# Performance work log

Hardware: AMD Instinct MI355X
Metric: run time of the kernel (lower is better)

The kernel has to match this reference:

```python
import jax, jax.numpy as jnp
import numpy as np


def setup_inputs() -> dict:
    key = jax.random.key(0)
    ks = jax.random.split(key, 8)
    B, C, N = 4, 64, 32768
    d = C // 8
    inp = {
        "x": jax.random.normal(ks[0], (B, C, N), dtype=jnp.float32),
        "Wq": jax.random.normal(ks[1], (d, C), dtype=jnp.float32) * 0.1,
        "bq": jax.random.normal(ks[2], (d,), dtype=jnp.float32) * 0.1,
        "Wk": jax.random.normal(ks[3], (d, C), dtype=jnp.float32) * 0.1,
        "bk": jax.random.normal(ks[4], (d,), dtype=jnp.float32) * 0.1,
        "Wv": jax.random.normal(ks[5], (C, C), dtype=jnp.float32) * 0.1,
        "bv": jax.random.normal(ks[6], (C,), dtype=jnp.float32) * 0.1,
        # nn.Parameter(torch.zeros(1)) in the original; nonzero here so the
        # attention branch actually contributes to the output.
        "gamma": jax.random.normal(ks[7], (1,), dtype=jnp.float32) * 0.1,
        "window_size": 512,
        "stride": 256,
        "pooling_factor": 2,
    }
    return inp


def reference(x, Wq, bq, Wk, bk, Wv, bv, gamma, window_size, stride, pooling_factor):
    B, C, N = x.shape
    # conv1x1 projections are pointwise -> apply once on the full signal
    q = jnp.einsum("dc,bcn->bdn", Wq, x) + bq[None, :, None]  # [B, d, N]
    k = jnp.einsum("dc,bcn->bdn", Wk, x) + bk[None, :, None]  # [B, d, N]
    v = jnp.einsum("ec,bcn->ben", Wv, x) + bv[None, :, None]  # [B, C, N]

    starts = jnp.arange(0, N - window_size + 1, stride)              # [W]
    idx = starts[:, None] + jnp.arange(window_size)[None, :]         # [W, ws]

    qw = q[:, :, idx]  # [B, d, W, ws]
    kw = k[:, :, idx]
    vw = v[:, :, idx]  # [B, C, W, ws]
    xw = x[:, :, idx]

    energy = jnp.einsum("bdwi,bdwj->bwij", qw, kw)                   # [B, W, ws, ws]
    attn = jax.nn.softmax(energy, axis=-1)
    # torch: bmm(v, attn^T) -> out[c,i] = sum_j v[c,j] * attn[i,j]
    out_local = jnp.einsum("bcwj,bwij->bcwi", vw, attn)              # [B, C, W, ws]

    contrib = gamma[0] * out_local + xw
    out = jnp.zeros_like(x).at[:, :, idx].add(contrib)               # overlap-add
    counts = jnp.zeros((N,), x.dtype).at[idx].add(1.0)               # overlap count
    out = out / counts[None, None, :]

    P = pooling_factor
    Np = (N // P) * P
    out = out[:, :, :Np].reshape(B, C, N // P, P).max(axis=-1)       # MaxPool1d(P)
    return out
```

## Files before the change

### kernel.cpp

```cpp
#include <hip/hip_runtime.h>
#include <hip/hip_bf16.h>

#define BB 4
#define CC 64
#define DD 8
#define NN 32768
#define WW 512
#define STR 256
#define NWIN 127
#define LOG2E 1.4426950408889634f

typedef short bf16x8 __attribute__((ext_vector_type(8)));
typedef float f32x4 __attribute__((ext_vector_type(4)));
typedef float f32x16 __attribute__((ext_vector_type(16)));

__device__ __forceinline__ unsigned int pack_bf16(float lo, float hi) {
    __hip_bfloat162 h = __float22bfloat162_rn(make_float2(lo, hi));
    unsigned int r; __builtin_memcpy(&r, &h, 4);
    return r;
}
__device__ __forceinline__ unsigned short to_bf16(float f) {
    __hip_bfloat16 h = __float2bfloat16(f);
    unsigned short r; __builtin_memcpy(&r, &h, 2);
    return r;
}
__device__ __forceinline__ float bf2f(unsigned short s) {
    union { unsigned int u; float f; } v; v.u = ((unsigned int)s) << 16;
    return v.f;
}
__device__ __forceinline__ float fast_exp2(float x) {
#if __has_builtin(__builtin_amdgcn_exp2f)
    return __builtin_amdgcn_exp2f(x);
#else
    float r; asm("v_exp_f32 %0, %1" : "=v"(r) : "v"(x)); return r;
#endif
}
__device__ __forceinline__ void plswap(unsigned int &x, unsigned int &y) {
    asm("v_permlane32_swap_b32 %0, %1" : "+v"(x), "+v"(y));
}
__device__ __forceinline__ bf16x8 pack8(float a0, float a1, float a2, float a3,
                                        float a4, float a5, float a6, float a7) {
    union { bf16x8 v; unsigned int u[4]; } r;
    r.u[0] = pack_bf16(a0, a1); r.u[1] = pack_bf16(a2, a3);
    r.u[2] = pack_bf16(a4, a5); r.u[3] = pack_bf16(a6, a7);
    return r.v;
}
__device__ __forceinline__ bf16x8 words4(unsigned int w0, unsigned int w1,
                                         unsigned int w2, unsigned int w3) {
    union { bf16x8 v; unsigned int u[4]; } r;
    r.u[0] = w0; r.u[1] = w1; r.u[2] = w2; r.u[3] = w3;
    return r.v;
}


__global__ __launch_bounds__(256) void qkv_kernel(
    const float* __restrict__ x,
    const float* __restrict__ Wq, const float* __restrict__ bq,
    const float* __restrict__ Wk, const float* __restrict__ bk,
    const float* __restrict__ Wv, const float* __restrict__ bv,
    unsigned short* __restrict__ qout, unsigned short* __restrict__ kout,
    unsigned short* __restrict__ vout)
{
    const int t = threadIdx.x;
    const int lane = t & 63, wv = t >> 6;
    const int a = lane & 15, g = lane >> 4;

    bf16x8 wf[5][2];
    #pragma unroll
    for (int T = 0; T < 5; ++T) {
        const float* wrow;
        float scale = 1.f;
        if (T == 0) {
            if (a < 8) { wrow = Wq + a*CC; scale = LOG2E; }
            else       { wrow = Wk + (a-8)*CC; }
        } else {
            wrow = Wv + ((T-1)*16 + a)*CC;
        }
        #pragma unroll
        for (int h = 0; h < 2; ++h) {
            float4 w0 = *(const float4*)(wrow + h*32 + g*8);
            float4 w1 = *(const float4*)(wrow + h*32 + g*8 + 4);
            wf[T][h] = pack8(w0.x*scale, w0.y*scale, w0.z*scale, w0.w*scale,
                             w1.x*scale, w1.y*scale, w1.z*scale, w1.w*scale);
        }
    }
    f32x4 bias[5];
    {
        const int r = g*4;
        #pragma unroll
        for (int u = 0; u < 4; ++u) {
            int rr = r + u;
            bias[0][u] = (rr < 8) ? bq[rr]*LOG2E : bk[rr-8];
        }
        #pragma unroll
        for (int T = 1; T < 5; ++T)
            #pragma unroll
            for (int u = 0; u < 4; ++u)
                bias[T][u] = bv[(T-1)*16 + r + u];
    }

    const int wave_id = blockIdx.x*4 + wv;
    #pragma unroll 1
    for (int it = 0; it < 2; ++it) {
        const int chunk = wave_id + it*4096;
        const int b = chunk >> 11;
        const int n0 = (chunk & 2047) * 16;
        const int n = n0 + a;
        const float* xcol = x + (size_t)b*CC*NN + n;

        float xv0[8], xv1[8];
        #pragma unroll
        for (int u = 0; u < 8; ++u) xv0[u] = xcol[(size_t)(g*8 + u)*NN];
        #pragma unroll
        for (int u = 0; u < 8; ++u) xv1[u] = xcol[(size_t)(32 + g*8 + u)*NN];
        bf16x8 xb0 = pack8(xv0[0],xv0[1],xv0[2],xv0[3],xv0[4],xv0[5],xv0[6],xv0[7]);
        bf16x8 xb1 = pack8(xv1[0],xv1[1],xv1[2],xv1[3],xv1[4],xv1[5],xv1[6],xv1[7]);

        f32x4 acc[5];
        #pragma unroll
        for (int T = 0; T < 5; ++T) {
            acc[T] = __builtin_amdgcn_mfma_f32_16x16x32_bf16(wf[T][0], xb0, bias[T], 0, 0, 0);
            acc[T] = __builtin_amdgcn_mfma_f32_16x16x32_bf16(wf[T][1], xb1, acc[T], 0, 0, 0);
        }

        {
            unsigned int lo = pack_bf16(acc[0][0], acc[0][1]);
            unsigned int hi = pack_bf16(acc[0][2], acc[0][3]);
            unsigned short* base = ((g < 2) ? qout : kout) + ((size_t)b*NN + n)*8 + (g & 1)*4;
            *(int2*)base = make_int2((int)lo, (int)hi);
        }
        unsigned short* vtb = vout + (((size_t)b*1024 + (n>>5))*4 + ((n>>3)&3))*512 + (n&7);
        #pragma unroll
        for (int T = 1; T < 5; ++T) {
            #pragma unroll
            for (int u = 0; u < 4; ++u) {
                const int e = (T-1)*16 + g*4 + u;
                vtb[e*8] = to_bf16(acc[T][u]);
            }
        }
    }
}

__global__ __launch_bounds__(128, 4) void attn_kernel(
    const unsigned short* __restrict__ qg, const unsigned short* __restrict__ kg,
    const unsigned short* __restrict__ vg,
    unsigned short* __restrict__ accE, unsigned short* __restrict__ accO)
{
    const int t = threadIdx.x;
    const int lane = t & 63, wv = t >> 6;
    const int l31 = lane & 31, hi = lane >> 5;
    int bid = (blockIdx.x & 7)*508 + (blockIdx.x >> 3);
    const int oct = bid & 7; bid >>= 3;
    const int w = bid % NWIN, b = bid / NWIN;
    const int nwin = STR * w;
    const int i0 = oct*64 + wv*32;

    const unsigned short* qbase = qg + ((size_t)b*NN + nwin + i0)*8;
    const unsigned short* kbase = kg + ((size_t)b*NN + nwin)*8;
    const unsigned short* vt = vg + (((size_t)b*1024 + 8*w)*4 + 2*hi)*512 + (size_t)l31*8;

    const bf16x8 zf = {};
    bf16x8 qf;
    {
        bf16x8 raw = *(const bf16x8*)(qbase + (size_t)l31*8);
        qf = hi ? zf : raw;
    }

    f32x16 acc[2] = {};
    float2 rsum2 = make_float2(0.f, 0.f);

    bf16x8 kc = *(const bf16x8*)(kbase + (size_t)l31*8);

    #pragma unroll 2
    for (int jt = 0; jt < 16; ++jt) {
        bf16x8 kn = kc;
        if (jt < 15) kn = *(const bf16x8*)(kbase + (size_t)(jt*32 + 32 + l31)*8);
        bf16x8 vc[2][2];
        #pragma unroll
        for (int ct = 0; ct < 2; ++ct)
            #pragma unroll
            for (int sl = 0; sl < 2; ++sl)
                vc[ct][sl] = *(const bf16x8*)(vt + (size_t)(jt*4 + sl*2)*512 + ct*256);

        const f32x16 z16 = {};
        f32x16 E = __builtin_amdgcn_mfma_f32_32x32x16_bf16(kc, qf, z16, 0, 0, 0);
        #pragma unroll
        for (int r = 0; r < 16; ++r) E[r] = fast_exp2(E[r]);
        float2 s0 = make_float2(E[0],  E[1])  + make_float2(E[2],  E[3]);
        float2 s1 = make_float2(E[4],  E[5])  + make_float2(E[6],  E[7]);
        float2 s2 = make_float2(E[8],  E[9])  + make_float2(E[10], E[11]);
        float2 s3 = make_float2(E[12], E[13]) + make_float2(E[14], E[15]);
        rsum2 += (s0 + s1) + (s2 + s3);
        unsigned int wd[8];
        #pragma unroll
        for (int tw = 0; tw < 8; ++tw) wd[tw] = pack_bf16(E[2*tw], E[2*tw+1]);
        unsigned int F0 = wd[0], F2 = wd[2]; plswap(F0, F2);
        unsigned int F1 = wd[1], F3 = wd[3]; plswap(F1, F3);
        unsigned int G0 = wd[4], G2 = wd[6]; plswap(G0, G2);
        unsigned int G1 = wd[5], G3 = wd[7]; plswap(G1, G3);
        bf16x8 pa0 = words4(F0, F1, F2, F3);
        bf16x8 pa1 = words4(G0, G1, G2, G3);
        #pragma unroll
        for (int ct = 0; ct < 2; ++ct) {
            acc[ct] = __builtin_amdgcn_mfma_f32_32x32x16_bf16(pa0, vc[ct][0], acc[ct], 0, 0, 0);
            acc[ct] = __builtin_amdgcn_mfma_f32_32x32x16_bf16(pa1, vc[ct][1], acc[ct], 0, 0, 0);
        }
        kc = kn;
    }

    float r = rsum2.x + rsum2.y;
    r += __shfl_xor(r, 32);
    const float inv = 1.f / r;
    f32x4 invv[4];
    #pragma unroll
    for (int g = 0; g < 4; ++g)
        #pragma unroll
        for (int u = 0; u < 4; ++u)
            invv[g][u] = __shfl(inv, 8*g + 4*hi + u);

    unsigned short* ob = ((w & 1) ? accO : accE)
        + ((size_t)b*1024 + ((nwin + i0) >> 5))*4*512 + 4*hi;
    #pragma unroll
    for (int ct = 0; ct < 2; ++ct) {
        unsigned short* cbase = ob + (ct*32 + l31)*8;
        #pragma unroll
        for (int g = 0; g < 4; ++g) {
            float a0 = acc[ct][4*g+0] * invv[g][0];
            float a1 = acc[ct][4*g+1] * invv[g][1];
            float a2 = acc[ct][4*g+2] * invv[g][2];
            float a3 = acc[ct][4*g+3] * invv[g][3];
            int2 pw = make_int2((int)pack_bf16(a0, a1), (int)pack_bf16(a2, a3));
            *(int2*)(cbase + (size_t)g*512) = pw;
        }
    }
}

__global__ __launch_bounds__(256) void final_kernel(
    const float* __restrict__ x,
    const unsigned short* __restrict__ accE, const unsigned short* __restrict__ accO,
    const float* __restrict__ gamma, float* __restrict__ out)
{
    const size_t tid = (size_t)blockIdx.x*256 + threadIdx.x;
    const size_t base = tid*8;
    const int n = (int)(base & (NN-1));
    const int c = (int)((base >> 15) & (CC-1));
    const int b = (int)(base >> 21);
    const float g = gamma[0];
    const size_t tadr = (((size_t)b*1024 + (n >> 5))*4 + ((n >> 3) & 3))*512 + c*8;

    float xv[8];
    *(float4*)&xv[0] = *(const float4*)&x[base];
    *(float4*)&xv[4] = *(const float4*)&x[base+4];
    int4 aeq = *(const int4*)&accE[tadr];
    const unsigned int* ae = (const unsigned int*)&aeq;

    float s[8];
    if (n >= STR && n < NN - STR) {
        int4 aoq = *(const int4*)&accO[tadr];
        const unsigned int* ao = (const unsigned int*)&aoq;
        #pragma unroll
        for (int u = 0; u < 4; ++u) {
            float e0 = bf2f((unsigned short)(ae[u] & 0xffff));
            float e1 = bf2f((unsigned short)(ae[u] >> 16));
            float o0 = bf2f((unsigned short)(ao[u] & 0xffff));
            float o1 = bf2f((unsigned short)(ao[u] >> 16));
            s[2*u]   = fmaf(g, (e0 + o0)*0.5f, xv[2*u]);
            s[2*u+1] = fmaf(g, (e1 + o1)*0.5f, xv[2*u+1]);
        }
    } else {
        #pragma unroll
        for (int u = 0; u < 4; ++u) {
            float e0 = bf2f((unsigned short)(ae[u] & 0xffff));
            float e1 = bf2f((unsigned short)(ae[u] >> 16));
            s[2*u]   = fmaf(g, e0, xv[2*u]);
            s[2*u+1] = fmaf(g, e1, xv[2*u+1]);
        }
    }
    float4 o = make_float4(fmaxf(s[0], s[1]), fmaxf(s[2], s[3]),
                           fmaxf(s[4], s[5]), fmaxf(s[6], s[7]));
    *(float4*)&out[tid*4] = o;
}

extern "C" void kernel_launch(void* const* d_in, const int* in_sizes, int n_in,
                              void* d_out, int out_size, void* d_ws, size_t ws_size,
                              hipStream_t stream)
{
    const float* x    = (const float*)d_in[0];
    const float* Wq   = (const float*)d_in[1];
    const float* bq   = (const float*)d_in[2];
    const float* Wk   = (const float*)d_in[3];
    const float* bk   = (const float*)d_in[4];
    const float* Wv   = (const float*)d_in[5];
    const float* bv   = (const float*)d_in[6];
    const float* gamma= (const float*)d_in[7];

    unsigned short* q    = (unsigned short*)d_ws;
    unsigned short* k    = q + (size_t)BB*NN*DD;
    unsigned short* v    = k + (size_t)BB*NN*DD;
    unsigned short* accE = v + (size_t)BB*CC*NN;
    unsigned short* accO = accE + (size_t)BB*CC*NN;
    float* out = (float*)d_out;

    qkv_kernel<<<1024, 256, 0, stream>>>(x, Wq, bq, Wk, bk, Wv, bv, q, k, v);
    attn_kernel<<<BB*NWIN*8, 128, 0, stream>>>(q, k, v, accE, accO);
    final_kernel<<<BB*CC*NN/8/256, 256, 0, stream>>>(x, accE, accO, gamma, out);
}
```

Baseline: 71.90 us.

## Merge overlapping window contributions inside attention kernel into single output buffer

The attention kernel is remapped so each block owns a 256-position output segment and runs up to two window passes, the previous and current windows, averaging their results in registers before writing. This removes the separate even and odd window buffers and the extra read of the second buffer in the final kernel, cutting global memory traffic. The cost is a serialized second pass per block, fewer blocks (2048 instead of 4064) and some extra registers to hold the first pass. The first result is also rounded to bf16 before the sum, which slightly changes numerics.

```diff
diff --git a/kernel.cpp b/kernel.cpp
--- a/kernel.cpp
+++ b/kernel.cpp
@@ -143,74 +143,79 @@
 
 __global__ __launch_bounds__(128, 4) void attn_kernel(
     const unsigned short* __restrict__ qg, const unsigned short* __restrict__ kg,
-    const unsigned short* __restrict__ vg,
-    unsigned short* __restrict__ accE, unsigned short* __restrict__ accO)
+    const unsigned short* __restrict__ vg, unsigned short* __restrict__ accT)
 {
     const int t = threadIdx.x;
     const int lane = t & 63, wv = t >> 6;
     const int l31 = lane & 31, hi = lane >> 5;
-    int bid = (blockIdx.x & 7)*508 + (blockIdx.x >> 3);
-    const int oct = bid & 7; bid >>= 3;
-    const int w = bid % NWIN, b = bid / NWIN;
-    const int nwin = STR * w;
-    const int i0 = oct*64 + wv*32;
-
-    const unsigned short* qbase = qg + ((size_t)b*NN + nwin + i0)*8;
-    const unsigned short* kbase = kg + ((size_t)b*NN + nwin)*8;
-    const unsigned short* vt = vg + (((size_t)b*1024 + 8*w)*4 + 2*hi)*512 + (size_t)l31*8;
+    int bid = (blockIdx.x & 7)*256 + (blockIdx.x >> 3);
+    const int q4 = bid & 3; bid >>= 2;
+    const int seg = bid & 127;
+    const int b = bid >> 7;
+    const int i0 = seg*256 + q4*64 + wv*32;
 
     const bf16x8 zf = {};
     bf16x8 qf;
     {
-        bf16x8 raw = *(const bf16x8*)(qbase + (size_t)l31*8);
+        bf16x8 raw = *(const bf16x8*)(qg + ((size_t)b*NN + i0 + l31)*8);
         qf = hi ? zf : raw;
     }
 
-    f32x16 acc[2] = {};
-    float2 rsum2 = make_float2(0.f, 0.f);
-
-    bf16x8 kc = *(const bf16x8*)(kbase + (size_t)l31*8);
-
-    #pragma unroll 2
-    for (int jt = 0; jt < 16; ++jt) {
-        bf16x8 kn = kc;
-        if (jt < 15) kn = *(const bf16x8*)(kbase + (size_t)(jt*32 + 32 + l31)*8);
-        bf16x8 vc[2][2];
-        #pragma unroll
-        for (int ct = 0; ct < 2; ++ct)
-            #pragma unroll
-            for (int sl = 0; sl < 2; ++sl)
-                vc[ct][sl] = *(const bf16x8*)(vt + (size_t)(jt*4 + sl*2)*512 + ct*256);
-
-        const f32x16 z16 = {};
-        f32x16 E = __builtin_amdgcn_mfma_f32_32x32x16_bf16(kc, qf, z16, 0, 0, 0);
-        #pragma unroll
-        for (int r = 0; r < 16; ++r) E[r] = fast_exp2(E[r]);
-        float2 s0 = make_float2(E[0],  E[1])  + make_float2(E[2],  E[3]);
-        float2 s1 = make_float2(E[4],  E[5])  + make_float2(E[6],  E[7]);
-        float2 s2 = make_float2(E[8],  E[9])  + make_float2(E[10], E[11]);
-        float2 s3 = make_float2(E[12], E[13]) + make_float2(E[14], E[15]);
-        rsum2 += (s0 + s1) + (s2 + s3);
-        unsigned int wd[8];
-        #pragma unroll
-        for (int tw = 0; tw < 8; ++tw) wd[tw] = pack_bf16(E[2*tw], E[2*tw+1]);
-        unsigned int F0 = wd[0], F2 = wd[2]; plswap(F0, F2);
-        unsigned int F1 = wd[1], F3 = wd[3]; plswap(F1, F3);
-        unsigned int G0 = wd[4], G2 = wd[6]; plswap(G0, G2);
-        unsigned int G1 = wd[5], G3 = wd[7]; plswap(G1, G3);
-        bf16x8 pa0 = words4(F0, F1, F2, F3);
-        bf16x8 pa1 = words4(G0, G1, G2, G3);
-        #pragma unroll
-        for (int ct = 0; ct < 2; ++ct) {
-            acc[ct] = __builtin_amdgcn_mfma_f32_32x32x16_bf16(pa0, vc[ct][0], acc[ct], 0, 0, 0);
-            acc[ct] = __builtin_amdgcn_mfma_f32_32x32x16_bf16(pa1, vc[ct][1], acc[ct], 0, 0, 0);
-        }
-        kc = kn;
-    }
-
-    float r = rsum2.x + rsum2.y;
-    r += __shfl_xor(r, 32);
-    const float inv = 1.f / r;
+    const bool dual = (seg > 0) && (seg < 127);
+    const int w0 = (seg > 0) ? seg - 1 : 0;
+
+    f32x16 acc[2];
+    float rs;
+
+    auto run_pass = [&](int wseg) {
+        const unsigned short* kb = kg + ((size_t)b*NN + (size_t)wseg*STR)*8;
+        const unsigned short* vt = vg + (((size_t)b*1024 + 8*wseg)*4 + 2*hi)*512 + (size_t)l31*8;
+        acc[0] = f32x16{}; acc[1] = f32x16{};
+        float2 rsum2 = make_float2(0.f, 0.f);
+        bf16x8 kc = *(const bf16x8*)(kb + (size_t)l31*8);
+        #pragma unroll 2
+        for (int jt = 0; jt < 16; ++jt) {
+            bf16x8 kn = kc;
+            if (jt < 15) kn = *(const bf16x8*)(kb + (size_t)(jt*32 + 32 + l31)*8);
+            bf16x8 vc[2][2];
+            #pragma unroll
+            for (int ct = 0; ct < 2; ++ct)
+                #pragma unroll
+                for (int sl = 0; sl < 2; ++sl)
+                    vc[ct][sl] = *(const bf16x8*)(vt + (size_t)(jt*4 + sl*2)*512 + ct*256);
+
+            const f32x16 z16 = {};
+            f32x16 E = __builtin_amdgcn_mfma_f32_32x32x16_bf16(kc, qf, z16, 0, 0, 0);
+            #pragma unroll
+            for (int r = 0; r < 16; ++r) E[r] = fast_exp2(E[r]);
+            float2 s0 = make_float2(E[0],  E[1])  + make_float2(E[2],  E[3]);
+            float2 s1 = make_float2(E[4],  E[5])  + make_float2(E[6],  E[7]);
+            float2 s2 = make_float2(E[8],  E[9])  + make_float2(E[10], E[11]);
+            float2 s3 = make_float2(E[12], E[13]) + make_float2(E[14], E[15]);
+            rsum2 += (s0 + s1) + (s2 + s3);
+            unsigned int wd[8];
+            #pragma unroll
+            for (int tw = 0; tw < 8; ++tw) wd[tw] = pack_bf16(E[2*tw], E[2*tw+1]);
+            unsigned int F0 = wd[0], F2 = wd[2]; plswap(F0, F2);
+            unsigned int F1 = wd[1], F3 = wd[3]; plswap(F1, F3);
+            unsigned int G0 = wd[4], G2 = wd[6]; plswap(G0, G2);
+            unsigned int G1 = wd[5], G3 = wd[7]; plswap(G1, G3);
+            bf16x8 pa0 = words4(F0, F1, F2, F3);
+            bf16x8 pa1 = words4(G0, G1, G2, G3);
+            #pragma unroll
+            for (int ct = 0; ct < 2; ++ct) {
+                acc[ct] = __builtin_amdgcn_mfma_f32_32x32x16_bf16(pa0, vc[ct][0], acc[ct], 0, 0, 0);
+                acc[ct] = __builtin_amdgcn_mfma_f32_32x32x16_bf16(pa1, vc[ct][1], acc[ct], 0, 0, 0);
+            }
+            kc = kn;
+        }
+        float r = rsum2.x + rsum2.y;
+        r += __shfl_xor(r, 32);
+        rs = r;
+    };
+
+    run_pass(w0);
+    float inv = 1.f / rs;
     f32x4 invv[4];
     #pragma unroll
     for (int g = 0; g < 4; ++g)
@@ -218,8 +223,26 @@
         for (int u = 0; u < 4; ++u)
             invv[g][u] = __shfl(inv, 8*g + 4*hi + u);
 
-    unsigned short* ob = ((w & 1) ? accO : accE)
-        + ((size_t)b*1024 + ((nwin + i0) >> 5))*4*512 + 4*hi;
+    unsigned int packA[2][8];
+    if (dual) {
+        #pragma unroll
+        for (int ct = 0; ct < 2; ++ct)
+            #pragma unroll
+            for (int g = 0; g < 4; ++g) {
+                packA[ct][2*g]   = pack_bf16(acc[ct][4*g+0]*invv[g][0], acc[ct][4*g+1]*invv[g][1]);
+                packA[ct][2*g+1] = pack_bf16(acc[ct][4*g+2]*invv[g][2], acc[ct][4*g+3]*invv[g][3]);
+            }
+        run_pass(seg);
+        inv = 1.f / rs;
+        #pragma unroll
+        for (int g = 0; g < 4; ++g)
+            #pragma unroll
+            for (int u = 0; u < 4; ++u)
+                invv[g][u] = __shfl(inv, 8*g + 4*hi + u);
+    }
+
+    const float sc = dual ? 0.5f : 1.f;
+    unsigned short* ob = accT + ((size_t)b*1024 + (i0 >> 5))*4*512 + 4*hi;
     #pragma unroll
     for (int ct = 0; ct < 2; ++ct) {
         unsigned short* cbase = ob + (ct*32 + l31)*8;
@@ -229,15 +252,20 @@
             float a1 = acc[ct][4*g+1] * invv[g][1];
             float a2 = acc[ct][4*g+2] * invv[g][2];
             float a3 = acc[ct][4*g+3] * invv[g][3];
-            int2 pw = make_int2((int)pack_bf16(a0, a1), (int)pack_bf16(a2, a3));
+            if (dual) {
+                a0 += bf2f((unsigned short)(packA[ct][2*g]   & 0xffff));
+                a1 += bf2f((unsigned short)(packA[ct][2*g]   >> 16));
+                a2 += bf2f((unsigned short)(packA[ct][2*g+1] & 0xffff));
+                a3 += bf2f((unsigned short)(packA[ct][2*g+1] >> 16));
+            }
+            int2 pw = make_int2((int)pack_bf16(a0*sc, a1*sc), (int)pack_bf16(a2*sc, a3*sc));
             *(int2*)(cbase + (size_t)g*512) = pw;
         }
     }
 }
 
 __global__ __launch_bounds__(256) void final_kernel(
-    const float* __restrict__ x,
-    const unsigned short* __restrict__ accE, const unsigned short* __restrict__ accO,
+    const float* __restrict__ x, const unsigned short* __restrict__ accT,
     const float* __restrict__ gamma, float* __restrict__ out)
 {
     const size_t tid = (size_t)blockIdx.x*256 + threadIdx.x;
@@ -251,30 +279,16 @@
     float xv[8];
     *(float4*)&xv[0] = *(const float4*)&x[base];
     *(float4*)&xv[4] = *(const float4*)&x[base+4];
-    int4 aeq = *(const int4*)&accE[tadr];
+    int4 aeq = *(const int4*)&accT[tadr];
     const unsigned int* ae = (const unsigned int*)&aeq;
 
     float s[8];
-    if (n >= STR && n < NN - STR) {
-        int4 aoq = *(const int4*)&accO[tadr];
-        const unsigned int* ao = (const unsigned int*)&aoq;
-        #pragma unroll
-        for (int u = 0; u < 4; ++u) {
-            float e0 = bf2f((unsigned short)(ae[u] & 0xffff));
-            float e1 = bf2f((unsigned short)(ae[u] >> 16));
-            float o0 = bf2f((unsigned short)(ao[u] & 0xffff));
-            float o1 = bf2f((unsigned short)(ao[u] >> 16));
-            s[2*u]   = fmaf(g, (e0 + o0)*0.5f, xv[2*u]);
-            s[2*u+1] = fmaf(g, (e1 + o1)*0.5f, xv[2*u+1]);
-        }
-    } else {
-        #pragma unroll
-        for (int u = 0; u < 4; ++u) {
-            float e0 = bf2f((unsigned short)(ae[u] & 0xffff));
-            float e1 = bf2f((unsigned short)(ae[u] >> 16));
-            s[2*u]   = fmaf(g, e0, xv[2*u]);
-            s[2*u+1] = fmaf(g, e1, xv[2*u+1]);
-        }
+    #pragma unroll
+    for (int u = 0; u < 4; ++u) {
+        float e0 = bf2f((unsigned short)(ae[u] & 0xffff));
+        float e1 = bf2f((unsigned short)(ae[u] >> 16));
+        s[2*u]   = fmaf(g, e0, xv[2*u]);
+        s[2*u+1] = fmaf(g, e1, xv[2*u+1]);
     }
     float4 o = make_float4(fmaxf(s[0], s[1]), fmaxf(s[2], s[3]),
                            fmaxf(s[4], s[5]), fmaxf(s[6], s[7]));
@@ -297,11 +311,10 @@
     unsigned short* q    = (unsigned short*)d_ws;
     unsigned short* k    = q + (size_t)BB*NN*DD;
     unsigned short* v    = k + (size_t)BB*NN*DD;
-    unsigned short* accE = v + (size_t)BB*CC*NN;
-    unsigned short* accO = accE + (size_t)BB*CC*NN;
+    unsigned short* accT = v + (size_t)BB*CC*NN;
     float* out = (float*)d_out;
 
     qkv_kernel<<<1024, 256, 0, stream>>>(x, Wq, bq, Wk, bk, Wv, bv, q, k, v);
-    attn_kernel<<<BB*NWIN*8, 128, 0, stream>>>(q, k, v, accE, accO);
-    final_kernel<<<BB*CC*NN/8/256, 256, 0, stream>>>(x, accE, accO, gamma, out);
-}
+    attn_kernel<<<2048, 128, 0, stream>>>(q, k, v, accT);
+    final_kernel<<<BB*CC*NN/8/256, 256, 0, stream>>>(x, accT, gamma, out);
+}
```

Result: slower. 77.17 us (+7.3%).
